# Optimization experiments

Hardware: AMD Instinct MI355X
Metric: run time of the kernel (lower is better)

Reference implementation:

```python
import jax, jax.numpy as jnp
import numpy as np


@jax.custom_vjp
def binary_act(x):
    # sign forward, straight-through (clipped) backward, matching BinaryActivation
    return jnp.sign(x)

def _ba_fwd(x):
    return jnp.sign(x), x

def _ba_bwd(x, g):
    return (jnp.where((x >= -1.0) & (x <= 1.0), g, 0.0),)

binary_act.defvjp(_ba_fwd, _ba_bwd)


def conv2d(x, w, b, pad, groups):
    # x: NCHW, w: OIHW
    y = jax.lax.conv_general_dilated(
        x, w, window_strides=(1, 1), padding=[(pad, pad), (pad, pad)],
        feature_group_count=groups,
        dimension_numbers=("NCHW", "OIHW", "NCHW"))
    return y + b[None, :, None, None]


def bconv(x, w, b, pad, groups):
    # Binary_conv2d: weights and bias binarized via sign (no STE on weights in torch either)
    return conv2d(x, jnp.sign(w), jnp.sign(b), pad, groups)


def maxpool2(x):
    return jax.lax.reduce_window(x, -jnp.inf, jax.lax.max,
                                 (1, 1, 2, 2), (1, 1, 2, 2), "VALID")


def setup_inputs() -> dict:
    key = jax.random.key(0)
    ks = jax.random.split(key, 14)
    d = {}
    d["x"] = jax.random.normal(ks[0], (1024, 3, 32, 32), dtype=jnp.float32)
    # conv1: depthwise 3x3 (groups=3) then 1x1 3->128
    d["w1_dw"] = jax.random.normal(ks[1], (3, 1, 3, 3), dtype=jnp.float32) * 0.1
    d["b1_dw"] = jax.random.normal(ks[2], (3,), dtype=jnp.float32) * 0.1
    d["w1_pw"] = jax.random.normal(ks[3], (128, 3, 1, 1), dtype=jnp.float32) * 0.1
    d["b1_pw"] = jax.random.normal(ks[4], (128,), dtype=jnp.float32) * 0.1
    # conv2: depthwise 3x3 (groups=128) then 1x1 128->256
    d["w2_dw"] = jax.random.normal(ks[5], (128, 1, 3, 3), dtype=jnp.float32) * 0.1
    d["b2_dw"] = jax.random.normal(ks[6], (128,), dtype=jnp.float32) * 0.1
    d["w2_pw"] = jax.random.normal(ks[7], (256, 128, 1, 1), dtype=jnp.float32) * 0.1
    d["b2_pw"] = jax.random.normal(ks[8], (256,), dtype=jnp.float32) * 0.1
    # fc layers (full precision weights, sign applied to fc1 output only)
    d["fc1_w"] = jax.random.normal(ks[9], (1024, 256 * 8 * 8), dtype=jnp.float32) * (1.0 / np.sqrt(256 * 8 * 8))
    d["fc1_b"] = jnp.zeros((1024,), dtype=jnp.float32)
    d["fc2_w"] = jax.random.normal(ks[10], (10, 1024), dtype=jnp.float32) * (1.0 / np.sqrt(1024.0))
    d["fc2_b"] = jnp.zeros((10,), dtype=jnp.float32)
    return d


def reference(x, w1_dw, b1_dw, w1_pw, b1_pw, w2_dw, b2_dw, w2_pw, b2_pw,
              fc1_w, fc1_b, fc2_w, fc2_b):
    h = bconv(x, w1_dw, b1_dw, pad=1, groups=3)        # [B,3,32,32]
    h = bconv(h, w1_pw, b1_pw, pad=0, groups=1)        # [B,128,32,32]
    h = maxpool2(binary_act(h))                        # [B,128,16,16]
    h = bconv(h, w2_dw, b2_dw, pad=1, groups=128)      # [B,128,16,16]
    h = bconv(h, w2_pw, b2_pw, pad=0, groups=1)        # [B,256,16,16]
    h = maxpool2(binary_act(h))                        # [B,256,8,8]
    h = h.reshape(h.shape[0], -1)                      # [B,16384]
    h = binary_act(h @ fc1_w.T + fc1_b)                # [B,1024]
    return h @ fc2_w.T + fc2_b                         # [B,10]
```

## Files before the change

### kernel.cpp

```cpp
#include <hip/hip_runtime.h>


__device__ __forceinline__ int fsign(float v)  { return (v > 0.f) - (v < 0.f); }
__device__ __forceinline__ int dsign(double v) { return (v > 0.0) - (v < 0.0); }

typedef int v4i __attribute__((ext_vector_type(4)));

__device__ __forceinline__ void async16(const signed char* g, signed char* l) {
    __builtin_amdgcn_global_load_lds(
        (const __attribute__((address_space(1))) void*)g,
        (__attribute__((address_space(3))) void*)l, 16, 0, 0);
}

__global__ void kprep2(const float* __restrict__ w2pw, const float* __restrict__ b2pw,
                       signed char* __restrict__ w2s, int* __restrict__ b2adj)
{
    int o = blockIdx.x * 64 + threadIdx.x;
    int rs = 0;
    for (int cq = 0; cq < 32; cq++) {
        float4 w = *(const float4*)(w2pw + (size_t)o * 128 + cq * 4);
        int s0 = fsign(w.x), s1 = fsign(w.y), s2 = fsign(w.z), s3 = fsign(w.w);
        rs += s0 + s1 + s2 + s3;
        int pk = (s0 & 0xff) | ((s1 & 0xff) << 8) | ((s2 & 0xff) << 16) | ((s3 & 0xff) << 24);
        *(int*)(w2s + (size_t)o * 128 + cq * 4) = pk;
    }
    b2adj[o] = fsign(b2pw[o]) - 32 * rs;
}

__global__ __launch_bounds__(256, 4) void k13b_fused(
    const float* __restrict__ x,
    const float* __restrict__ w1dw, const float* __restrict__ b1dw,
    const float* __restrict__ w1pw, const float* __restrict__ b1pw,
    const float* __restrict__ w2dw, const float* __restrict__ b2dw,
    const signed char* __restrict__ w2s, const int* __restrict__ b2adj,
    signed char* __restrict__ hT2,
    const float* __restrict__ fc1w, signed char* __restrict__ BL)
{
    __shared__ __align__(16) signed char Ps[32768];
    __shared__ __align__(16) signed char sw4[1152];
    __shared__ signed char sdb2[128];
    __shared__ int sb2adj[256];
    __shared__ float sdw[27], sbdw[3];
    __shared__ unsigned char spidx[128];

    int t = threadIdx.x, l = t & 63, wid = t >> 6;
    int n = blockIdx.x;

    if (t < 27) sdw[t] = (float)fsign(w1dw[t]);
    if (t < 3)  sbdw[t] = (float)fsign(b1dw[t]);
    if (t < 128) {
        int b0 = w1pw[t * 3 + 0] > 0.f;
        int b1 = w1pw[t * 3 + 1] > 0.f;
        int b2 = w1pw[t * 3 + 2] > 0.f;
        int b3 = b1pw[t] > 0.f;
        spidx[t] = (unsigned char)(b0 | (b1 << 1) | (b2 << 2) | (b3 << 3));
    }
    for (int i = t; i < 1152; i += 256) {
        int c = i & 127, tap = i >> 7;
        sw4[tap * 128 + c] = (signed char)fsign(w2dw[c * 9 + tap]);
    }
    if (t < 128) sdb2[t] = (signed char)(fsign(b2dw[t]) + 1);
    sb2adj[t] = b2adj[t];
    __syncthreads();

    {
        int px = t & 15, py = t >> 4;
        double h[3][4];
        const float* xb = x + (size_t)n * 3 * 1024;
        #pragma unroll
        for (int c = 0; c < 3; c++) {
            const float* xc = xb + c * 1024;
            #pragma unroll
            for (int dy = 0; dy < 2; dy++)
            #pragma unroll
            for (int dx = 0; dx < 2; dx++) {
                int y = 2 * py + dy, xx = 2 * px + dx;
                double acc = (double)sbdw[c];
                #pragma unroll
                for (int ky = 0; ky < 3; ky++) {
                    int yy = y + ky - 1;
                    if (yy < 0 || yy > 31) continue;
                    #pragma unroll
                    for (int kx = 0; kx < 3; kx++) {
                        int xxx = xx + kx - 1;
                        if (xxx < 0 || xxx > 31) continue;
                        acc += (double)sdw[c * 9 + ky * 3 + kx] * (double)xc[yy * 32 + xxx];
                    }
                }
                h[c][dy * 2 + dx] = acc;
            }
        }

        double tv[4][4];
        #pragma unroll
        for (int q = 0; q < 4; q++) {
            double u = h[0][q] + h[1][q];
            double v = h[0][q] - h[1][q];
            tv[0][q] = v - h[2][q];
            tv[1][q] = u - h[2][q];
            tv[2][q] = v + h[2][q];
            tv[3][q] = u + h[2][q];
        }
        int mpack = 0;
        #pragma unroll
        for (int bp = 0; bp < 4; bp++) {
            int mxP = -2, mnP = 2, mxM = -2, mnM = 2;
            #pragma unroll
            for (int q = 0; q < 4; q++) {
                int sP = dsign(tv[bp][q] + 1.0);
                int sM = dsign(tv[bp][q] - 1.0);
                mxP = max(mxP, sP); mnP = min(mnP, sP);
                mxM = max(mxM, sM); mnM = min(mnM, sM);
            }
            int pat1 = 1 | (bp << 1);
            int pat0 = (~pat1) & 7;
            mpack |= (mxP + 1)   << (2 * (pat1 | 8));
            mpack |= (mxM + 1)   << (2 * pat1);
            mpack |= ((-mnM) + 1) << (2 * (pat0 | 8));
            mpack |= ((-mnP) + 1) << (2 * pat0);
        }

        signed char* prow = Ps + t * 128;
        const int* pint = (const int*)spidx;
        for (int ob = 0; ob < 32; ob++) {
            int pw = pint[ob];
            int cur = 0;
            #pragma unroll
            for (int e = 0; e < 4; e++) {
                int pi = (pw >> (8 * e)) & 15;
                int mv = ((mpack >> (pi * 2)) & 3) - 1;
                cur |= (mv & 0xff) << (8 * e);
            }
            int ad = (((ob >> 2) ^ (t & 7)) << 4) + (ob & 3) * 4;
            *(int*)(prow + ad) = cur;
        }
    }
    __syncthreads();

    int frow = l & 15;

    v4i af[4][2];
    #pragma unroll
    for (int ks = 0; ks < 2; ks++) {
        int c0 = ks * 64 + (l >> 4) * 16;
        int cc = c0 >> 4;
        int4 w4[9];
        #pragma unroll
        for (int tap = 0; tap < 9; tap++)
            w4[tap] = *(const int4*)&sw4[tap * 128 + c0];
        int4 sdbv = *(const int4*)&sdb2[c0];

        #pragma unroll
        for (int i = 0; i < 4; i++) {
            int r = (wid * 4 + i) * 16 + frow;
            int py = r >> 5, px2 = (r >> 2) & 7, dy = (r >> 1) & 1, dx = r & 1;
            int y = 2 * py + dy, xq = 2 * px2 + dx;
            int4 cnt = (int4){0, 0, 0, 0};
            #pragma unroll
            for (int ky = 0; ky < 3; ky++) {
                int yy = y + ky - 1;
                int yc = min(max(yy, 0), 15);
                #pragma unroll
                for (int kx = 0; kx < 3; kx++) {
                    int xx2 = xq + kx - 1;
                    int xc = min(max(xx2, 0), 15);
                    int inb = ((yy == yc) && (xx2 == xc)) ? 0x01010101 : 0;
                    int p = yc * 16 + xc;
                    int4 v = *(const int4*)&Ps[p * 128 + ((cc ^ (p & 7)) * 16)];
                    int4 w = w4[ky * 3 + kx];
                    cnt.x += ((v.x ^ w.x) >> 1) & inb;
                    cnt.y += ((v.y ^ w.y) >> 1) & inb;
                    cnt.z += ((v.z ^ w.z) >> 1) & inb;
                    cnt.w += ((v.w ^ w.w) >> 1) & inb;
                }
            }
            int valid = (1 + (y > 0) + (y < 15)) * (1 + (xq > 0) + (xq < 15));
            int mb = (valid + 31) * 0x01010101;
            int4 u;
            u.x = sdbv.x + mb - (cnt.x + cnt.x);
            u.y = sdbv.y + mb - (cnt.y + cnt.y);
            u.z = sdbv.z + mb - (cnt.z + cnt.z);
            u.w = sdbv.w + mb - (cnt.w + cnt.w);
            af[i][ks] = (v4i){u.x, u.y, u.z, u.w};
        }
    }
    __syncthreads();

    for (int oc = 0; oc < 4; oc++) {
        v4i acc[4][4];
        #pragma unroll
        for (int i = 0; i < 4; i++)
            #pragma unroll
            for (int jt = 0; jt < 4; jt++) acc[i][jt] = (v4i){0, 0, 0, 0};

        #pragma unroll
        for (int ks = 0; ks < 2; ks++) {
            v4i bf[4];
            #pragma unroll
            for (int jt = 0; jt < 4; jt++)
                bf[jt] = *(const v4i*)(w2s + (size_t)(oc * 64 + jt * 16 + frow) * 128
                                       + ks * 64 + (l >> 4) * 16);
            __builtin_amdgcn_s_setprio(1);
            #pragma unroll
            for (int i = 0; i < 4; i++)
                #pragma unroll
                for (int jt = 0; jt < 4; jt++)
                    acc[i][jt] = __builtin_amdgcn_mfma_i32_16x16x64_i8(af[i][ks], bf[jt], acc[i][jt], 0, 0, 0);
            __builtin_amdgcn_s_setprio(0);
        }

        signed char* Osp = Ps + oc * 5120;
        #pragma unroll
        for (int jt = 0; jt < 4; jt++) {
            int o_l = jt * 16 + frow;
            int bia = sb2adj[oc * 64 + o_l];
            #pragma unroll
            for (int i = 0; i < 4; i++) {
                int mx = -2;
                #pragma unroll
                for (int rr = 0; rr < 4; rr++) {
                    int p = acc[i][jt][rr] + bia;
                    int s = (p > 0) - (p < 0);
                    mx = s > mx ? s : mx;
                }
                int pp = (wid * 4 + i) * 4 + (l >> 4);
                Osp[o_l * 80 + pp] = (signed char)mx;
            }
        }
    }
    __syncthreads();

    #pragma unroll
    for (int oc = 0; oc < 4; oc++)
        *(int4*)&hT2[(size_t)n * 16384 + oc * 4096 + t * 16]
            = *(const int4*)&Ps[oc * 5120 + (t >> 2) * 80 + (t & 3) * 16];

    {
        const float* fr = fc1w + (size_t)n * 16384;
        #pragma unroll 4
        for (int kb = 0; kb < 16; kb++) {
            int k0 = kb * 1024 + t * 4;
            float4 w = *(const float4*)(fr + k0);
            float we[4] = {w.x, w.y, w.z, w.w};
            int out[4] = {0, 0, 0, 0};
            #pragma unroll
            for (int e = 0; e < 4; e++) {
                int q = (int)rint((double)we[e] * 4294967296.0);
                q = min(max(q, -266338304), 266338304);
                int d0 = ((q + 64) & 127) - 64; q = (q - d0) >> 7;
                int d1 = ((q + 64) & 127) - 64; q = (q - d1) >> 7;
                int d2 = ((q + 64) & 127) - 64; q = (q - d2) >> 7;
                int d3 = q;
                out[0] |= (d0 & 0xff) << (8 * e);
                out[1] |= (d1 & 0xff) << (8 * e);
                out[2] |= (d2 & 0xff) << (8 * e);
                out[3] |= (d3 & 0xff) << (8 * e);
            }
            #pragma unroll
            for (int m = 0; m < 4; m++)
                *(int*)(BL + (size_t)(n * 4 + m) * 16384 + k0) = out[m];
        }
    }
}

__global__ __launch_bounds__(512, 2) void k4a_fc1(
    const signed char* __restrict__ hT2, const signed char* __restrict__ BL,
    double* __restrict__ Pd)
{
    __shared__ __align__(16) signed char smem[98304];
    int t = threadIdx.x, l = t & 63, wid = t >> 6;
    int nb0 = blockIdx.y * 128, jb0 = blockIdx.x * 256;
    int kh = blockIdx.z, k0 = kh * 8192;
    int ksw = wid >> 2;
    int wn0 = ((wid >> 1) & 1) * 64, wj0 = (wid & 1) * 128;

    int srow = l >> 3;
    int sseg = ((l & 7) ^ srow) * 16;
    const signed char* gA = hT2 + (size_t)(nb0 + wid * 16 + srow) * 16384 + k0 + sseg;
    const signed char* gB = BL  + (size_t)(jb0 + wid * 32 + srow) * 16384 + k0 + sseg;

    v4i acc[4][8];
    #pragma unroll
    for (int i = 0; i < 4; i++)
        #pragma unroll
        for (int q = 0; q < 8; q++) acc[i][q] = (v4i){0, 0, 0, 0};

    {
        signed char* As = smem;
        signed char* Bs = smem + 16384;
        #pragma unroll
        for (int c = 0; c < 2; c++)
            async16(gA + (size_t)c * 8 * 16384, As + (wid * 16 + c * 8) * 128);
        #pragma unroll
        for (int c = 0; c < 4; c++)
            async16(gB + (size_t)c * 8 * 16384, Bs + (wid * 32 + c * 8) * 128);
    }

    int sw = (((ksw * 4) + (l >> 4)) ^ (l & 7)) * 16;

    for (int it = 0; it < 64; it++) {
        __syncthreads();
        if (it + 1 < 64) {
            int kt = (it + 1) * 128;
            signed char* As = smem + ((it + 1) & 1) * 49152;
            signed char* Bs = As + 16384;
            #pragma unroll
            for (int c = 0; c < 2; c++)
                async16(gA + (size_t)c * 8 * 16384 + kt, As + (wid * 16 + c * 8) * 128);
            #pragma unroll
            for (int c = 0; c < 4; c++)
                async16(gB + (size_t)c * 8 * 16384 + kt, Bs + (wid * 32 + c * 8) * 128);
        }
        const signed char* As = smem + (it & 1) * 49152;
        const signed char* Bs = As + 16384;
        v4i af[4], bf[8];
        #pragma unroll
        for (int i = 0; i < 4; i++)
            af[i] = *(const v4i*)&As[(wn0 + i * 16 + (l & 15)) * 128 + sw];
        #pragma unroll
        for (int q = 0; q < 8; q++)
            bf[q] = *(const v4i*)&Bs[(wj0 + q * 16 + (l & 15)) * 128 + sw];
        #pragma unroll
        for (int i = 0; i < 4; i++)
            #pragma unroll
            for (int q = 0; q < 8; q++)
                acc[i][q] = __builtin_amdgcn_mfma_i32_16x16x64_i8(af[i], bf[q], acc[i][q], 0, 0, 0);
    }

    __syncthreads();
    int* S = (int*)smem;
    #pragma unroll
    for (int h = 0; h < 2; h++) {
        if (h) __syncthreads();
        if (ksw == 0 && wn0 == h * 64) {
            #pragma unroll
            for (int i = 0; i < 4; i++)
                #pragma unroll
                for (int q = 0; q < 8; q++)
                    #pragma unroll
                    for (int rr = 0; rr < 4; rr++)
                        S[(i * 16 + (l >> 4) * 4 + rr) * 256 + (wj0 + q * 16 + (l & 15))]
                            = acc[i][q][rr];
        }
        __syncthreads();
        if (ksw == 1 && wn0 == h * 64) {
            #pragma unroll
            for (int i = 0; i < 4; i++)
                #pragma unroll
                for (int q = 0; q < 8; q++)
                    #pragma unroll
                    for (int rr = 0; rr < 4; rr++)
                        S[(i * 16 + (l >> 4) * 4 + rr) * 256 + (wj0 + q * 16 + (l & 15))]
                            += acc[i][q][rr];
        }
        __syncthreads();
        #pragma unroll
        for (int e = 0; e < 8; e++) {
            int idx = t * 8 + e;
            int n_l = idx >> 6, j_l = idx & 63;
            int4 s = *(const int4*)&S[n_l * 256 + j_l * 4];
            double val = (double)s.x + 128.0 * (double)s.y
                       + 16384.0 * (double)s.z + 2097152.0 * (double)s.w;
            Pd[(size_t)kh * 1048576 + (size_t)(nb0 + h * 64 + n_l) * 1024
               + blockIdx.x * 64 + j_l] = val;
        }
    }
}

__global__ __launch_bounds__(256) void k45_comb_fc2(
    const double* __restrict__ Pd, const float* __restrict__ fc1b,
    const float* __restrict__ fc2w, const float* __restrict__ fc2b,
    float* __restrict__ out)
{
    __shared__ double sj[1024];
    __shared__ double pw[4][10];
    int t = threadIdx.x, n = blockIdx.x;
    const double SCALE = 1.0 / 4294967296.0;

    #pragma unroll
    for (int rep = 0; rep < 4; rep++) {
        int j = rep * 256 + t;
        double v = Pd[(size_t)n * 1024 + j] + Pd[1048576 + (size_t)n * 1024 + j];
        double p = v * SCALE + (double)fc1b[j];
        sj[j] = (double)((p > 0.0) - (p < 0.0));
    }
    __syncthreads();

    int j0 = t * 4;
    double s0 = sj[j0], s1 = sj[j0 + 1], s2 = sj[j0 + 2], s3 = sj[j0 + 3];
    double acc[10];
    #pragma unroll
    for (int m = 0; m < 10; m++) {
        float4 w = *(const float4*)(fc2w + (size_t)m * 1024 + j0);
        acc[m] = s0 * (double)w.x + s1 * (double)w.y + s2 * (double)w.z + s3 * (double)w.w;
    }
    #pragma unroll
    for (int off = 32; off > 0; off >>= 1)
        #pragma unroll
        for (int m = 0; m < 10; m++)
            acc[m] += __shfl_down(acc[m], off);
    if ((t & 63) == 0)
        #pragma unroll
        for (int m = 0; m < 10; m++) pw[t >> 6][m] = acc[m];
    __syncthreads();
    if (t < 10)
        out[n * 10 + t] = (float)(pw[0][t] + pw[1][t] + pw[2][t] + pw[3][t] + (double)fc2b[t]);
}

__global__ __launch_bounds__(512) void k4_fc1_mfma(
    const signed char* __restrict__ hT2, const signed char* __restrict__ BL,
    const float* __restrict__ fc1b, signed char* __restrict__ hs)
{
    __shared__ __align__(16) signed char smem[65536];
    int t = threadIdx.x, l = t & 63, wid = t >> 6;
    int nb0 = blockIdx.y * 128, jb0 = blockIdx.x * 128;
    int wn0 = (wid >> 1) * 32;
    int wj0 = (wid & 1) * 64;

    int srow = l >> 3;
    int sseg = ((l & 7) ^ srow) * 16;
    const signed char* gA = hT2 + (size_t)(nb0 + wid * 16 + srow) * 16384 + sseg;
    const signed char* gB = BL  + (size_t)(jb0 + wid * 16 + srow) * 16384 + sseg;

    v4i acc[2][4];
    #pragma unroll
    for (int i = 0; i < 2; i++)
        #pragma unroll
        for (int q = 0; q < 4; q++) acc[i][q] = (v4i){0, 0, 0, 0};

    {
        signed char* As = smem;
        signed char* Bs = smem + 16384;
        #pragma unroll
        for (int i = 0; i < 2; i++) {
            async16(gA + (size_t)i * 8 * 16384, As + (wid * 16 + i * 8) * 128);
            async16(gB + (size_t)i * 8 * 16384, Bs + (wid * 16 + i * 8) * 128);
        }
    }

    for (int it = 0; it < 128; it++) {
        __syncthreads();
        if (it + 1 < 128) {
            int kt = (it + 1) * 128;
            signed char* As = smem + ((it + 1) & 1) * 32768;
            signed char* Bs = As + 16384;
            #pragma unroll
            for (int i = 0; i < 2; i++) {
                async16(gA + (size_t)i * 8 * 16384 + kt, As + (wid * 16 + i * 8) * 128);
                async16(gB + (size_t)i * 8 * 16384 + kt, Bs + (wid * 16 + i * 8) * 128);
            }
        }
        const signed char* As = smem + (it & 1) * 32768;
        const signed char* Bs = As + 16384;
        #pragma unroll
        for (int ks = 0; ks < 2; ks++) {
            int sw = (((ks * 4) + (l >> 4)) ^ (l & 7)) * 16;
            v4i af[2], bf[4];
            #pragma unroll
            for (int i = 0; i < 2; i++)
                af[i] = *(const v4i*)&As[(wn0 + i * 16 + (l & 15)) * 128 + sw];
            #pragma unroll
            for (int q = 0; q < 4; q++)
                bf[q] = *(const v4i*)&Bs[(wj0 + q * 16 + (l & 15)) * 128 + sw];
            #pragma unroll
            for (int i = 0; i < 2; i++)
                #pragma unroll
                for (int q = 0; q < 4; q++)
                    acc[i][q] = __builtin_amdgcn_mfma_i32_16x16x64_i8(af[i], bf[q], acc[i][q], 0, 0, 0);
        }
    }

    __syncthreads();
    int* S = (int*)smem;
    #pragma unroll
    for (int i = 0; i < 2; i++)
        #pragma unroll
        for (int q = 0; q < 4; q++)
            #pragma unroll
            for (int rr = 0; rr < 4; rr++) {
                int n_l  = wn0 + i * 16 + (l >> 4) * 4 + rr;
                int jm_l = wj0 + q * 16 + (l & 15);
                S[n_l * 128 + jm_l] = acc[i][q][rr];
            }
    __syncthreads();

    const double SCALE = 1.0 / 4294967296.0;
    #pragma unroll
    for (int i = 0; i < 8; i++) {
        int idx = t * 8 + i;
        int n_l = idx >> 5, j_l = idx & 31;
        int4 s = *(const int4*)&S[n_l * 128 + j_l * 4];
        double val = (double)s.x + 128.0 * (double)s.y
                   + 16384.0 * (double)s.z + 2097152.0 * (double)s.w;
        int j = blockIdx.x * 32 + j_l;
        double p = val * SCALE + (double)fc1b[j];
        hs[(size_t)(nb0 + n_l) * 1024 + j] = (signed char)((p > 0.0) - (p < 0.0));
    }
}

__global__ void k5_fc2(const signed char* __restrict__ hs,
                       const float* __restrict__ fc2w, const float* __restrict__ fc2b,
                       float* __restrict__ out)
{
    int idx = blockIdx.x * 64 + threadIdx.x;
    if (idx >= 10240) return;
    int n = idx / 10, m = idx - n * 10;
    const signed char* hr = hs + (size_t)n * 1024;
    const float* wr = fc2w + (size_t)m * 1024;
    double acc = (double)fc2b[m];
    for (int jb = 0; jb < 1024; jb += 16) {
        int4 hv = *(const int4*)(hr + jb);
        int wd[4] = {hv.x, hv.y, hv.z, hv.w};
        #pragma unroll
        for (int u = 0; u < 4; u++)
            #pragma unroll
            for (int e = 0; e < 4; e++)
                acc += (double)(signed char)(wd[u] >> (8 * e)) * (double)wr[jb + u * 4 + e];
    }
    out[idx] = (float)acc;
}

extern "C" void kernel_launch(void* const* d_in, const int* in_sizes, int n_in,
                              void* d_out, int out_size, void* d_ws, size_t ws_size,
                              hipStream_t stream)
{
    const float* x    = (const float*)d_in[0];
    const float* w1dw = (const float*)d_in[1];
    const float* b1dw = (const float*)d_in[2];
    const float* w1pw = (const float*)d_in[3];
    const float* b1pw = (const float*)d_in[4];
    const float* w2dw = (const float*)d_in[5];
    const float* b2dw = (const float*)d_in[6];
    const float* w2pw = (const float*)d_in[7];
    const float* b2pw = (const float*)d_in[8];
    const float* fc1w = (const float*)d_in[9];
    const float* fc1b = (const float*)d_in[10];
    const float* fc2w = (const float*)d_in[11];
    const float* fc2b = (const float*)d_in[12];
    float* out = (float*)d_out;

    char* ws = (char*)d_ws;
    signed char* hT2      = (signed char*)(ws + 67108864);
    signed char* w2s      = (signed char*)(ws + 83886080);
    int*         b2adj    = (int*)(ws + 83886080 + 32768);
    signed char* BL       = (signed char*)(ws);
    signed char* hs       = (signed char*)(ws + 83886080 + 1048576);
    double*      Pd       = (double*)(ws + 84934656);
    bool split = ws_size >= (size_t)84934656 + 16777216;

    hipLaunchKernelGGL(kprep2,     dim3(4),    dim3(64),  0, stream,
                       w2pw, b2pw, w2s, b2adj);
    hipLaunchKernelGGL(k13b_fused, dim3(1024), dim3(256), 0, stream,
                       x, w1dw, b1dw, w1pw, b1pw, w2dw, b2dw, w2s, b2adj, hT2,
                       fc1w, BL);
    if (split) {
        hipLaunchKernelGGL(k4a_fc1,      dim3(16, 8, 2), dim3(512), 0, stream,
                           hT2, BL, Pd);
        hipLaunchKernelGGL(k45_comb_fc2, dim3(1024),     dim3(256), 0, stream,
                           Pd, fc1b, fc2w, fc2b, out);
    } else {
        hipLaunchKernelGGL(k4_fc1_mfma, dim3(32, 8), dim3(512), 0, stream,
                           hT2, BL, fc1b, hs);
        hipLaunchKernelGGL(k5_fc2,      dim3(160),   dim3(64),  0, stream,
                           hs, fc2w, fc2b, out);
    }
}
```

Measured before the change: 295.1 us.

## Double fused conv kernel block size to 512 threads, splitting per-thread work

The fused conv+binarize+pwconv kernel now runs 512 threads per block instead of 256. Each output pixel's depthwise stage is split across two lanes, which combine their max/min results with shuffles. Each wave handles half as many MFMA row tiles, and the store and fc1 weight-quantization loops are redistributed to match. This aims to raise parallelism and latency hiding within the fixed 1024-block grid, at the cost of more register pressure under the 512,8 launch bounds and some extra shuffle overhead.

```diff
diff --git a/kernel.cpp b/kernel.cpp
--- a/kernel.cpp
+++ b/kernel.cpp
@@ -27,7 +27,7 @@
     b2adj[o] = fsign(b2pw[o]) - 32 * rs;
 }
 
-__global__ __launch_bounds__(256, 4) void k13b_fused(
+__global__ __launch_bounds__(512, 8) void k13c_fused(
     const float* __restrict__ x,
     const float* __restrict__ w1dw, const float* __restrict__ b1dw,
     const float* __restrict__ w1pw, const float* __restrict__ b1pw,
@@ -55,23 +55,23 @@
         int b3 = b1pw[t] > 0.f;
         spidx[t] = (unsigned char)(b0 | (b1 << 1) | (b2 << 2) | (b3 << 3));
     }
-    for (int i = t; i < 1152; i += 256) {
+    for (int i = t; i < 1152; i += 512) {
         int c = i & 127, tap = i >> 7;
         sw4[tap * 128 + c] = (signed char)fsign(w2dw[c * 9 + tap]);
     }
     if (t < 128) sdb2[t] = (signed char)(fsign(b2dw[t]) + 1);
-    sb2adj[t] = b2adj[t];
+    if (t < 256) sb2adj[t] = b2adj[t];
     __syncthreads();
 
     {
-        int px = t & 15, py = t >> 4;
-        double h[3][4];
+        int pix = t >> 1, half = t & 1;
+        int px = pix & 15, py = pix >> 4;
+        int dy = half;
+        double h[3][2];
         const float* xb = x + (size_t)n * 3 * 1024;
         #pragma unroll
         for (int c = 0; c < 3; c++) {
             const float* xc = xb + c * 1024;
-            #pragma unroll
-            for (int dy = 0; dy < 2; dy++)
             #pragma unroll
             for (int dx = 0; dx < 2; dx++) {
                 int y = 2 * py + dy, xx = 2 * px + dx;
@@ -87,13 +87,13 @@
                         acc += (double)sdw[c * 9 + ky * 3 + kx] * (double)xc[yy * 32 + xxx];
                     }
                 }
-                h[c][dy * 2 + dx] = acc;
-            }
-        }
-
-        double tv[4][4];
-        #pragma unroll
-        for (int q = 0; q < 4; q++) {
+                h[c][dx] = acc;
+            }
+        }
+
+        double tv[4][2];
+        #pragma unroll
+        for (int q = 0; q < 2; q++) {
             double u = h[0][q] + h[1][q];
             double v = h[0][q] - h[1][q];
             tv[0][q] = v - h[2][q];
@@ -106,12 +106,16 @@
         for (int bp = 0; bp < 4; bp++) {
             int mxP = -2, mnP = 2, mxM = -2, mnM = 2;
             #pragma unroll
-            for (int q = 0; q < 4; q++) {
+            for (int q = 0; q < 2; q++) {
                 int sP = dsign(tv[bp][q] + 1.0);
                 int sM = dsign(tv[bp][q] - 1.0);
                 mxP = max(mxP, sP); mnP = min(mnP, sP);
                 mxM = max(mxM, sM); mnM = min(mnM, sM);
             }
+            mxP = max(mxP, __shfl_xor(mxP, 1));
+            mnP = min(mnP, __shfl_xor(mnP, 1));
+            mxM = max(mxM, __shfl_xor(mxM, 1));
+            mnM = min(mnM, __shfl_xor(mnM, 1));
             int pat1 = 1 | (bp << 1);
             int pat0 = (~pat1) & 7;
             mpack |= (mxP + 1)   << (2 * (pat1 | 8));
@@ -120,9 +124,10 @@
             mpack |= ((-mnP) + 1) << (2 * pat0);
         }
 
-        signed char* prow = Ps + t * 128;
+        signed char* prow = Ps + pix * 128;
         const int* pint = (const int*)spidx;
-        for (int ob = 0; ob < 32; ob++) {
+        for (int ob2 = 0; ob2 < 16; ob2++) {
+            int ob = half * 16 + ob2;
             int pw = pint[ob];
             int cur = 0;
             #pragma unroll
@@ -131,7 +136,7 @@
                 int mv = ((mpack >> (pi * 2)) & 3) - 1;
                 cur |= (mv & 0xff) << (8 * e);
             }
-            int ad = (((ob >> 2) ^ (t & 7)) << 4) + (ob & 3) * 4;
+            int ad = (((ob >> 2) ^ (pix & 7)) << 4) + (ob & 3) * 4;
             *(int*)(prow + ad) = cur;
         }
     }
@@ -139,7 +144,7 @@
 
     int frow = l & 15;
 
-    v4i af[4][2];
+    v4i af[2][2];
     #pragma unroll
     for (int ks = 0; ks < 2; ks++) {
         int c0 = ks * 64 + (l >> 4) * 16;
@@ -151,8 +156,8 @@
         int4 sdbv = *(const int4*)&sdb2[c0];
 
         #pragma unroll
-        for (int i = 0; i < 4; i++) {
-            int r = (wid * 4 + i) * 16 + frow;
+        for (int i = 0; i < 2; i++) {
+            int r = (wid * 2 + i) * 16 + frow;
             int py = r >> 5, px2 = (r >> 2) & 7, dy = (r >> 1) & 1, dx = r & 1;
             int y = 2 * py + dy, xq = 2 * px2 + dx;
             int4 cnt = (int4){0, 0, 0, 0};
@@ -187,9 +192,9 @@
     __syncthreads();
 
     for (int oc = 0; oc < 4; oc++) {
-        v4i acc[4][4];
-        #pragma unroll
-        for (int i = 0; i < 4; i++)
+        v4i acc[2][4];
+        #pragma unroll
+        for (int i = 0; i < 2; i++)
             #pragma unroll
             for (int jt = 0; jt < 4; jt++) acc[i][jt] = (v4i){0, 0, 0, 0};
 
@@ -202,7 +207,7 @@
                                        + ks * 64 + (l >> 4) * 16);
             __builtin_amdgcn_s_setprio(1);
             #pragma unroll
-            for (int i = 0; i < 4; i++)
+            for (int i = 0; i < 2; i++)
                 #pragma unroll
                 for (int jt = 0; jt < 4; jt++)
                     acc[i][jt] = __builtin_amdgcn_mfma_i32_16x16x64_i8(af[i][ks], bf[jt], acc[i][jt], 0, 0, 0);
@@ -215,7 +220,7 @@
             int o_l = jt * 16 + frow;
             int bia = sb2adj[oc * 64 + o_l];
             #pragma unroll
-            for (int i = 0; i < 4; i++) {
+            for (int i = 0; i < 2; i++) {
                 int mx = -2;
                 #pragma unroll
                 for (int rr = 0; rr < 4; rr++) {
@@ -223,7 +228,7 @@
                     int s = (p > 0) - (p < 0);
                     mx = s > mx ? s : mx;
                 }
-                int pp = (wid * 4 + i) * 4 + (l >> 4);
+                int pp = (wid * 2 + i) * 4 + (l >> 4);
                 Osp[o_l * 80 + pp] = (signed char)mx;
             }
         }
@@ -231,15 +236,18 @@
     __syncthreads();
 
     #pragma unroll
-    for (int oc = 0; oc < 4; oc++)
-        *(int4*)&hT2[(size_t)n * 16384 + oc * 4096 + t * 16]
-            = *(const int4*)&Ps[oc * 5120 + (t >> 2) * 80 + (t & 3) * 16];
+    for (int rep = 0; rep < 2; rep++) {
+        int id = rep * 512 + t;
+        int oc = id >> 8, ii = id & 255;
+        *(int4*)&hT2[(size_t)n * 16384 + oc * 4096 + ii * 16]
+            = *(const int4*)&Ps[oc * 5120 + (ii >> 2) * 80 + (ii & 3) * 16];
+    }
 
     {
         const float* fr = fc1w + (size_t)n * 16384;
-        #pragma unroll 4
-        for (int kb = 0; kb < 16; kb++) {
-            int k0 = kb * 1024 + t * 4;
+        #pragma unroll 2
+        for (int kb = 0; kb < 8; kb++) {
+            int k0 = kb * 2048 + t * 4;
             float4 w = *(const float4*)(fr + k0);
             float we[4] = {w.x, w.y, w.z, w.w};
             int out[4] = {0, 0, 0, 0};
@@ -550,7 +558,7 @@
 
     hipLaunchKernelGGL(kprep2,     dim3(4),    dim3(64),  0, stream,
                        w2pw, b2pw, w2s, b2adj);
-    hipLaunchKernelGGL(k13b_fused, dim3(1024), dim3(256), 0, stream,
+    hipLaunchKernelGGL(k13c_fused, dim3(1024), dim3(512), 0, stream,
                        x, w1dw, b1dw, w1pw, b1pw, w2dw, b2dw, w2s, b2adj, hT2,
                        fc1w, BL);
     if (split) {
```

Result: slower. 403.5 us (+36.7%).
